# Optimization experiments

Hardware: AMD Instinct MI355X
Metric: run time of the kernel (lower is better)

The kernel has to match this reference:

```python
import jax, jax.numpy as jnp
import numpy as np

TAU = 0.1  # temperature (registered buffer, non-trainable)
EPS = 1e-12  # F.normalize eps


def setup_inputs() -> dict:
    key = jax.random.key(0)
    k1, k2 = jax.random.split(key)
    B, C = 4096, 512
    z1 = jax.random.normal(k1, (B, C), dtype=jnp.float32)
    z2 = jax.random.normal(k2, (B, C), dtype=jnp.float32)
    return {"z1": z1, "z2": z2}


def _l2_normalize(x):
    # matches F.normalize(p=2, dim=1): x / max(||x||, eps)
    n = jnp.sqrt(jnp.sum(x * x, axis=1, keepdims=True))
    return x / jnp.maximum(n, EPS)


def reference(z1, z2):
    B = z1.shape[0]
    N = 2 * B
    z = jnp.concatenate([_l2_normalize(z1), _l2_normalize(z2)], axis=0)  # [2B, C]
    # cosine similarity of unit vectors == dot product -> single GEMM
    S = jnp.exp((z @ z.T) / TAU)  # [2B, 2B]
    rows = jnp.arange(N)
    pos_cols = (rows + B) % N  # mask[r, c]=1 iff r == (c+B) mod 2B  <=> c == (r+B) mod 2B
    positive = S[rows, pos_cols]                 # [2B]
    # negatives = row sum over ~mask; note the original INCLUDES the diagonal
    negative = jnp.sum(S, axis=1) - positive     # [2B]
    pairs_loss = -jnp.log(positive / negative)   # [2B]
    loss = pairs_loss.reshape(2, B).sum(axis=0) / N  # [B]
    return loss.mean()  # reduce=True
```

## Files before the change

### kernel.cpp

```cpp
#include <hip/hip_runtime.h>
#include <hip/hip_bf16.h>


#define BDIM 4096
#define CDIM 512
#define NROWS 8192
#define NTILE 32
#define NBLK 528
#define NKT 8

typedef __attribute__((ext_vector_type(4))) float f32x4;
typedef __attribute__((ext_vector_type(8))) short bf16x8;

#define AS1 __attribute__((address_space(1)))
#define AS3 __attribute__((address_space(3)))

__device__ __forceinline__ unsigned short f2bf_rne(float x) {
    unsigned u = __float_as_uint(x);
    u += 0x7fffu + ((u >> 16) & 1u);
    return (unsigned short)(u >> 16);
}

__global__ __launch_bounds__(256) void normalize_kernel(
    const float* __restrict__ z1, const float* __restrict__ z2,
    unsigned short* __restrict__ zb, float* __restrict__ pos10,
    float* __restrict__ rowsum, float* __restrict__ out) {
    if (blockIdx.x == 0) {
#pragma unroll
        for (int i = 0; i < NROWS / 256; ++i) rowsum[i * 256 + threadIdx.x] = 0.f;
        if (threadIdx.x == 0) out[0] = 0.f;
    }
    const int w = threadIdx.x >> 6, lane = threadIdx.x & 63;
    const int r = blockIdx.x * 4 + w;
    const float4* p1 = (const float4*)(z1 + (size_t)r * CDIM);
    const float4* p2 = (const float4*)(z2 + (size_t)r * CDIM);
    float4 a0 = p1[lane], a1 = p1[64 + lane];
    float4 b0 = p2[lane], b1 = p2[64 + lane];
    float s1 = a0.x * a0.x + a0.y * a0.y + a0.z * a0.z + a0.w * a0.w +
               a1.x * a1.x + a1.y * a1.y + a1.z * a1.z + a1.w * a1.w;
    float s2 = b0.x * b0.x + b0.y * b0.y + b0.z * b0.z + b0.w * b0.w +
               b1.x * b1.x + b1.y * b1.y + b1.z * b1.z + b1.w * b1.w;
    float d = a0.x * b0.x + a0.y * b0.y + a0.z * b0.z + a0.w * b0.w +
              a1.x * b1.x + a1.y * b1.y + a1.z * b1.z + a1.w * b1.w;
#pragma unroll
    for (int m = 1; m < 64; m <<= 1) {
        s1 += __shfl_xor(s1, m, 64);
        s2 += __shfl_xor(s2, m, 64);
        d += __shfl_xor(d, m, 64);
    }
    const float n1 = fmaxf(sqrtf(s1), 1e-12f);
    const float n2 = fmaxf(sqrtf(s2), 1e-12f);
    const float i1 = 1.0f / n1, i2 = 1.0f / n2;
    ushort4 o;
    ushort4* q1 = (ushort4*)(zb + (size_t)r * CDIM);
    ushort4* q2 = (ushort4*)(zb + (size_t)(r + BDIM) * CDIM);
    o.x = f2bf_rne(a0.x * i1); o.y = f2bf_rne(a0.y * i1);
    o.z = f2bf_rne(a0.z * i1); o.w = f2bf_rne(a0.w * i1);
    q1[lane] = o;
    o.x = f2bf_rne(a1.x * i1); o.y = f2bf_rne(a1.y * i1);
    o.z = f2bf_rne(a1.z * i1); o.w = f2bf_rne(a1.w * i1);
    q1[64 + lane] = o;
    o.x = f2bf_rne(b0.x * i2); o.y = f2bf_rne(b0.y * i2);
    o.z = f2bf_rne(b0.z * i2); o.w = f2bf_rne(b0.w * i2);
    q2[lane] = o;
    o.x = f2bf_rne(b1.x * i2); o.y = f2bf_rne(b1.y * i2);
    o.z = f2bf_rne(b1.z * i2); o.w = f2bf_rne(b1.w * i2);
    q2[64 + lane] = o;
    if (lane == 0) pos10[r] = (d / (n1 * n2)) * 10.0f;
}

__global__ __launch_bounds__(512, 2) void simgemm_kernel(
    const unsigned short* __restrict__ Z, float* __restrict__ rowsum) {
    int by = 0, rem = blockIdx.x;
    while (rem >= NTILE - by) { rem -= NTILE - by; ++by; }
    const int bx = by + rem;
    const bool diag = (bx == by);

    __shared__ unsigned short lds[2][4][128 * 64];

    const int t = threadIdx.x;
    const int lane = t & 63, w = t >> 6;
    const int wr = w >> 2, wc = w & 3;

    f32x4 acc[8][4] = {};

    const int srow = t >> 3;
    const int scolb = (((t & 7) ^ ((t >> 3) & 7)) << 4);
    const char* Zb = (const char*)Z;
    const size_t apan = ((size_t)(by * 256) << 10);
    const size_t bpan = ((size_t)(bx * 256) << 10);

#define STG(T, J)                                                                \
    {                                                                            \
        const size_t pb_ = ((J) < 2 ? apan : bpan);                              \
        const char* g0_ = Zb + pb_ +                                             \
            ((size_t)((((J) & 1) * 128) + srow) << 10) + ((T) * 128) + scolb;    \
        char* d0_ = (char*)&lds[(T) & 1][J][0] + w * 1024;                       \
        __builtin_amdgcn_global_load_lds((const AS1 void*)g0_,                   \
                                         (AS3 void*)d0_, 16, 0, 0);              \
        __builtin_amdgcn_global_load_lds((const AS1 void*)(g0_ + (64 << 10)),    \
                                         (AS3 void*)(d0_ + 8192), 16, 0, 0);     \
    }

    STG(0, 2); STG(0, 3); STG(0, 0); STG(0, 1); STG(1, 2); STG(1, 0);
    asm volatile("s_waitcnt vmcnt(4)\n\ts_barrier" ::: "memory");

    const int arow = lane & 15;
    const int brow0 = (wc & 1) * 64;
    const int klo = (lane >> 4) << 4;
    const int swz = (lane & 7) << 4;

#pragma unroll
    for (int T = 0; T < NKT; ++T) {
        const int buf = T & 1;
        const char* Ab = (const char*)&lds[buf][wr][0];
        const char* Bb = (const char*)&lds[buf][2 + (wc >> 1)][0];
        if (T >= 1) {
            if (T < NKT - 1)
                asm volatile("s_waitcnt vmcnt(4)\n\ts_barrier" ::: "memory");
            else
                asm volatile("s_waitcnt vmcnt(0)\n\ts_barrier" ::: "memory");
        }

        bf16x8 af[4][2], bf[4][2];

#pragma unroll
        for (int mi = 0; mi < 4; ++mi)
#pragma unroll
            for (int kk = 0; kk < 2; ++kk)
                af[mi][kk] = *(const bf16x8*)(Ab + (mi * 16 + arow) * 128 +
                                              ((kk * 64 + klo) ^ swz));
#pragma unroll
        for (int ni = 0; ni < 2; ++ni)
#pragma unroll
            for (int kk = 0; kk < 2; ++kk)
                bf[ni][kk] = *(const bf16x8*)(Bb + (brow0 + ni * 16 + arow) * 128 +
                                              ((kk * 64 + klo) ^ swz));
        if (T + 1 < NKT) STG(T + 1, 3);
        asm volatile("s_barrier" ::: "memory");
        __builtin_amdgcn_s_setprio(1);
#pragma unroll
        for (int mi = 0; mi < 4; ++mi)
#pragma unroll
            for (int ni = 0; ni < 2; ++ni)
#pragma unroll
                for (int kk = 0; kk < 2; ++kk)
                    acc[mi][ni] = __builtin_amdgcn_mfma_f32_16x16x32_bf16(
                        af[mi][kk], bf[ni][kk], acc[mi][ni], 0, 0, 0);
        __builtin_amdgcn_s_setprio(0);
        asm volatile("s_waitcnt lgkmcnt(0)\n\ts_barrier" ::: "memory");

#pragma unroll
        for (int ni = 2; ni < 4; ++ni)
#pragma unroll
            for (int kk = 0; kk < 2; ++kk)
                bf[ni][kk] = *(const bf16x8*)(Bb + (brow0 + ni * 16 + arow) * 128 +
                                              ((kk * 64 + klo) ^ swz));
        if (T + 1 < NKT) STG(T + 1, 1);
        asm volatile("s_barrier" ::: "memory");
        __builtin_amdgcn_s_setprio(1);
#pragma unroll
        for (int mi = 0; mi < 4; ++mi)
#pragma unroll
            for (int ni = 2; ni < 4; ++ni)
#pragma unroll
                for (int kk = 0; kk < 2; ++kk)
                    acc[mi][ni] = __builtin_amdgcn_mfma_f32_16x16x32_bf16(
                        af[mi][kk], bf[ni][kk], acc[mi][ni], 0, 0, 0);
        __builtin_amdgcn_s_setprio(0);
        asm volatile("s_waitcnt lgkmcnt(0)\n\ts_barrier" ::: "memory");

#pragma unroll
        for (int mi = 0; mi < 4; ++mi)
#pragma unroll
            for (int kk = 0; kk < 2; ++kk)
                af[mi][kk] = *(const bf16x8*)(Ab + ((mi + 4) * 16 + arow) * 128 +
                                              ((kk * 64 + klo) ^ swz));
        if (T + 2 < NKT) STG(T + 2, 2);
        asm volatile("s_barrier" ::: "memory");
        __builtin_amdgcn_s_setprio(1);
#pragma unroll
        for (int mi = 0; mi < 4; ++mi)
#pragma unroll
            for (int ni = 0; ni < 2; ++ni)
#pragma unroll
                for (int kk = 0; kk < 2; ++kk)
                    acc[mi + 4][ni] = __builtin_amdgcn_mfma_f32_16x16x32_bf16(
                        af[mi][kk], bf[ni][kk], acc[mi + 4][ni], 0, 0, 0);
        __builtin_amdgcn_s_setprio(0);
        asm volatile("s_waitcnt lgkmcnt(0)\n\ts_barrier" ::: "memory");

        if (T + 2 < NKT) STG(T + 2, 0);
        asm volatile("s_barrier" ::: "memory");
        __builtin_amdgcn_s_setprio(1);
#pragma unroll
        for (int mi = 0; mi < 4; ++mi)
#pragma unroll
            for (int ni = 2; ni < 4; ++ni)
#pragma unroll
                for (int kk = 0; kk < 2; ++kk)
                    acc[mi + 4][ni] = __builtin_amdgcn_mfma_f32_16x16x32_bf16(
                        af[mi][kk], bf[ni][kk], acc[mi + 4][ni], 0, 0, 0);
        __builtin_amdgcn_s_setprio(0);
        asm volatile("s_waitcnt lgkmcnt(0)\n\ts_barrier" ::: "memory");
    }
#undef STG

    const float SC = 14.4269504088896340736f;
    const int g = lane >> 4;
    float cs[4] = {0.f, 0.f, 0.f, 0.f};
#pragma unroll
    for (int mi = 0; mi < 8; ++mi) {
        float rs0 = 0.f, rs1 = 0.f, rs2 = 0.f, rs3 = 0.f;
#pragma unroll
        for (int ni = 0; ni < 4; ++ni) {
            f32x4 a = acc[mi][ni];
            const float e0 = exp2f(a[0] * SC);
            const float e1 = exp2f(a[1] * SC);
            const float e2 = exp2f(a[2] * SC);
            const float e3 = exp2f(a[3] * SC);
            rs0 += e0; rs1 += e1; rs2 += e2; rs3 += e3;
            cs[ni] += (e0 + e1) + (e2 + e3);
        }
#pragma unroll
        for (int m = 1; m < 16; m <<= 1) {
            rs0 += __shfl_xor(rs0, m, 64);
            rs1 += __shfl_xor(rs1, m, 64);
            rs2 += __shfl_xor(rs2, m, 64);
            rs3 += __shfl_xor(rs3, m, 64);
        }
        if ((lane & 15) == 0) {
            const int rbase = by * 256 + wr * 128 + mi * 16 + g * 4;
            atomicAdd(&rowsum[rbase + 0], rs0);
            atomicAdd(&rowsum[rbase + 1], rs1);
            atomicAdd(&rowsum[rbase + 2], rs2);
            atomicAdd(&rowsum[rbase + 3], rs3);
        }
    }
    if (!diag) {
#pragma unroll
        for (int ni = 0; ni < 4; ++ni) {
            float c = cs[ni];
            c += __shfl_xor(c, 16, 64);
            c += __shfl_xor(c, 32, 64);
            if (lane < 16)
                atomicAdd(&rowsum[bx * 256 + wc * 64 + ni * 16 + lane], c);
        }
    }
}

__global__ __launch_bounds__(256) void finalize_kernel(
    const float* __restrict__ rowsum, const float* __restrict__ pos10,
    float* __restrict__ out) {
    __shared__ float sm[4];
    const int w = threadIdx.x >> 6, lane = threadIdx.x & 63;
    const int r = blockIdx.x * 256 + threadIdx.x;
    const float p10 = pos10[r];
    const float pos = expf(p10);
    float l = (logf(rowsum[r] - pos) - p10) +
              (logf(rowsum[r + BDIM] - pos) - p10);
#pragma unroll
    for (int m = 1; m < 64; m <<= 1) l += __shfl_xor(l, m, 64);
    if (lane == 0) sm[w] = l;
    __syncthreads();
    if (threadIdx.x == 0) {
        const float tot = sm[0] + sm[1] + sm[2] + sm[3];
        atomicAdd(out, tot * (1.0f / ((float)NROWS * (float)BDIM)));
    }
}

extern "C" void kernel_launch(void* const* d_in, const int* in_sizes, int n_in,
                              void* d_out, int out_size, void* d_ws, size_t ws_size,
                              hipStream_t stream) {
    const float* z1 = (const float*)d_in[0];
    const float* z2 = (const float*)d_in[1];
    float* out = (float*)d_out;
    unsigned short* zb = (unsigned short*)d_ws;
    float* rowsum = (float*)((char*)d_ws + (size_t)NROWS * CDIM * 2);
    float* pos10 = rowsum + NROWS;

    normalize_kernel<<<BDIM / 4, 256, 0, stream>>>(z1, z2, zb, pos10, rowsum, out);
    simgemm_kernel<<<NBLK, 512, 0, stream>>>(zb, rowsum);
    finalize_kernel<<<BDIM / 256, 256, 0, stream>>>(rowsum, pos10, out);
}
```

Measured before the change: 143.3 us.

## Split anti-diagonal tiles into quarter blocks and remap tile order for balance

```diff
diff --git a/kernel.cpp b/kernel.cpp
--- a/kernel.cpp
+++ b/kernel.cpp
@@ -6,8 +6,8 @@
 #define CDIM 512
 #define NROWS 8192
 #define NTILE 32
-#define NBLK 528
 #define NKT 8
+#define NBLK 576
 
 typedef __attribute__((ext_vector_type(4))) float f32x4;
 typedef __attribute__((ext_vector_type(8))) short bf16x8;
@@ -71,24 +71,36 @@
 
 __global__ __launch_bounds__(512, 2) void simgemm_kernel(
     const unsigned short* __restrict__ Z, float* __restrict__ rowsum) {
-    int by = 0, rem = blockIdx.x;
-    while (rem >= NTILE - by) { rem -= NTILE - by; ++by; }
-    const int bx = by + rem;
-    const bool diag = (bx == by);
-
     __shared__ unsigned short lds[2][4][128 * 64];
 
     const int t = threadIdx.x;
     const int lane = t & 63, w = t >> 6;
     const int wr = w >> 2, wc = w & 3;
-
-    f32x4 acc[8][4] = {};
-
     const int srow = t >> 3;
     const int scolb = (((t & 7) ^ ((t >> 3) & 7)) << 4);
     const char* Zb = (const char*)Z;
-    const size_t apan = ((size_t)(by * 256) << 10);
-    const size_t bpan = ((size_t)(bx * 256) << 10);
+    const float SC = 14.4269504088896340736f;
+    const int g = lane >> 4;
+    const int arow = lane & 15;
+    const int klo = (lane >> 4) << 4;
+    const int swz = (lane & 7) << 4;
+    const int bid = blockIdx.x;
+
+    if (bid < 512) {
+        const int fid = (bid & 7) * 64 + (bid >> 3);
+        int by = 0, rem = fid;
+        while (true) {
+            const int cnt = (NTILE - by) - (by <= 15 ? 1 : 0);
+            if (rem < cnt) break;
+            rem -= cnt; ++by;
+        }
+        int bx = by + rem;
+        if (by <= 15 && bx >= 31 - by) ++bx;
+        const bool diag = (bx == by);
+
+        f32x4 acc[8][4] = {};
+        const size_t apan = ((size_t)(by * 256) << 10);
+        const size_t bpan = ((size_t)(bx * 256) << 10);
 
 #define STG(T, J)                                                                \
     {                                                                            \
@@ -102,150 +114,220 @@
                                          (AS3 void*)(d0_ + 8192), 16, 0, 0);     \
     }
 
-    STG(0, 2); STG(0, 3); STG(0, 0); STG(0, 1); STG(1, 2); STG(1, 0);
-    asm volatile("s_waitcnt vmcnt(4)\n\ts_barrier" ::: "memory");
-
-    const int arow = lane & 15;
-    const int brow0 = (wc & 1) * 64;
-    const int klo = (lane >> 4) << 4;
-    const int swz = (lane & 7) << 4;
-
-#pragma unroll
-    for (int T = 0; T < NKT; ++T) {
-        const int buf = T & 1;
-        const char* Ab = (const char*)&lds[buf][wr][0];
-        const char* Bb = (const char*)&lds[buf][2 + (wc >> 1)][0];
-        if (T >= 1) {
-            if (T < NKT - 1)
-                asm volatile("s_waitcnt vmcnt(4)\n\ts_barrier" ::: "memory");
-            else
-                asm volatile("s_waitcnt vmcnt(0)\n\ts_barrier" ::: "memory");
-        }
-
-        bf16x8 af[4][2], bf[4][2];
-
-#pragma unroll
-        for (int mi = 0; mi < 4; ++mi)
-#pragma unroll
-            for (int kk = 0; kk < 2; ++kk)
-                af[mi][kk] = *(const bf16x8*)(Ab + (mi * 16 + arow) * 128 +
-                                              ((kk * 64 + klo) ^ swz));
-#pragma unroll
-        for (int ni = 0; ni < 2; ++ni)
-#pragma unroll
-            for (int kk = 0; kk < 2; ++kk)
-                bf[ni][kk] = *(const bf16x8*)(Bb + (brow0 + ni * 16 + arow) * 128 +
-                                              ((kk * 64 + klo) ^ swz));
-        if (T + 1 < NKT) STG(T + 1, 3);
-        asm volatile("s_barrier" ::: "memory");
-        __builtin_amdgcn_s_setprio(1);
-#pragma unroll
-        for (int mi = 0; mi < 4; ++mi)
+        STG(0, 2); STG(0, 3); STG(0, 0); STG(0, 1); STG(1, 2); STG(1, 0);
+        asm volatile("s_waitcnt vmcnt(4)\n\ts_barrier" ::: "memory");
+
+        const int brow0 = (wc & 1) * 64;
+#pragma unroll
+        for (int T = 0; T < NKT; ++T) {
+            const int buf = T & 1;
+            const char* Ab = (const char*)&lds[buf][wr][0];
+            const char* Bb = (const char*)&lds[buf][2 + (wc >> 1)][0];
+            if (T >= 1) {
+                if (T < NKT - 1)
+                    asm volatile("s_waitcnt vmcnt(4)\n\ts_barrier" ::: "memory");
+                else
+                    asm volatile("s_waitcnt vmcnt(0)\n\ts_barrier" ::: "memory");
+            }
+
+            bf16x8 af[4][2], bf[4][2];
+
+#pragma unroll
+            for (int mi = 0; mi < 4; ++mi)
+#pragma unroll
+                for (int kk = 0; kk < 2; ++kk)
+                    af[mi][kk] = *(const bf16x8*)(Ab + (mi * 16 + arow) * 128 +
+                                                  ((kk * 64 + klo) ^ swz));
 #pragma unroll
             for (int ni = 0; ni < 2; ++ni)
 #pragma unroll
                 for (int kk = 0; kk < 2; ++kk)
-                    acc[mi][ni] = __builtin_amdgcn_mfma_f32_16x16x32_bf16(
-                        af[mi][kk], bf[ni][kk], acc[mi][ni], 0, 0, 0);
-        __builtin_amdgcn_s_setprio(0);
-        asm volatile("s_waitcnt lgkmcnt(0)\n\ts_barrier" ::: "memory");
-
-#pragma unroll
-        for (int ni = 2; ni < 4; ++ni)
-#pragma unroll
-            for (int kk = 0; kk < 2; ++kk)
-                bf[ni][kk] = *(const bf16x8*)(Bb + (brow0 + ni * 16 + arow) * 128 +
-                                              ((kk * 64 + klo) ^ swz));
-        if (T + 1 < NKT) STG(T + 1, 1);
-        asm volatile("s_barrier" ::: "memory");
-        __builtin_amdgcn_s_setprio(1);
-#pragma unroll
-        for (int mi = 0; mi < 4; ++mi)
+                    bf[ni][kk] = *(const bf16x8*)(Bb + (brow0 + ni * 16 + arow) * 128 +
+                                                  ((kk * 64 + klo) ^ swz));
+            if (T + 1 < NKT) STG(T + 1, 3);
+            asm volatile("s_barrier" ::: "memory");
+            __builtin_amdgcn_s_setprio(1);
+#pragma unroll
+            for (int mi = 0; mi < 4; ++mi)
+#pragma unroll
+                for (int ni = 0; ni < 2; ++ni)
+#pragma unroll
+                    for (int kk = 0; kk < 2; ++kk)
+                        acc[mi][ni] = __builtin_amdgcn_mfma_f32_16x16x32_bf16(
+                            af[mi][kk], bf[ni][kk], acc[mi][ni], 0, 0, 0);
+            __builtin_amdgcn_s_setprio(0);
+            asm volatile("s_waitcnt lgkmcnt(0)\n\ts_barrier" ::: "memory");
+
 #pragma unroll
             for (int ni = 2; ni < 4; ++ni)
 #pragma unroll
                 for (int kk = 0; kk < 2; ++kk)
-                    acc[mi][ni] = __builtin_amdgcn_mfma_f32_16x16x32_bf16(
-                        af[mi][kk], bf[ni][kk], acc[mi][ni], 0, 0, 0);
-        __builtin_amdgcn_s_setprio(0);
-        asm volatile("s_waitcnt lgkmcnt(0)\n\ts_barrier" ::: "memory");
-
-#pragma unroll
-        for (int mi = 0; mi < 4; ++mi)
-#pragma unroll
-            for (int kk = 0; kk < 2; ++kk)
-                af[mi][kk] = *(const bf16x8*)(Ab + ((mi + 4) * 16 + arow) * 128 +
-                                              ((kk * 64 + klo) ^ swz));
-        if (T + 2 < NKT) STG(T + 2, 2);
-        asm volatile("s_barrier" ::: "memory");
-        __builtin_amdgcn_s_setprio(1);
-#pragma unroll
-        for (int mi = 0; mi < 4; ++mi)
-#pragma unroll
-            for (int ni = 0; ni < 2; ++ni)
+                    bf[ni][kk] = *(const bf16x8*)(Bb + (brow0 + ni * 16 + arow) * 128 +
+                                                  ((kk * 64 + klo) ^ swz));
+            if (T + 1 < NKT) STG(T + 1, 1);
+            asm volatile("s_barrier" ::: "memory");
+            __builtin_amdgcn_s_setprio(1);
+#pragma unroll
+            for (int mi = 0; mi < 4; ++mi)
+#pragma unroll
+                for (int ni = 2; ni < 4; ++ni)
+#pragma unroll
+                    for (int kk = 0; kk < 2; ++kk)
+                        acc[mi][ni] = __builtin_amdgcn_mfma_f32_16x16x32_bf16(
+                            af[mi][kk], bf[ni][kk], acc[mi][ni], 0, 0, 0);
+            __builtin_amdgcn_s_setprio(0);
+            asm volatile("s_waitcnt lgkmcnt(0)\n\ts_barrier" ::: "memory");
+
+#pragma unroll
+            for (int mi = 0; mi < 4; ++mi)
 #pragma unroll
                 for (int kk = 0; kk < 2; ++kk)
-                    acc[mi + 4][ni] = __builtin_amdgcn_mfma_f32_16x16x32_bf16(
-                        af[mi][kk], bf[ni][kk], acc[mi + 4][ni], 0, 0, 0);
-        __builtin_amdgcn_s_setprio(0);
-        asm volatile("s_waitcnt lgkmcnt(0)\n\ts_barrier" ::: "memory");
-
-        if (T + 2 < NKT) STG(T + 2, 0);
-        asm volatile("s_barrier" ::: "memory");
-        __builtin_amdgcn_s_setprio(1);
-#pragma unroll
-        for (int mi = 0; mi < 4; ++mi)
-#pragma unroll
-            for (int ni = 2; ni < 4; ++ni)
-#pragma unroll
-                for (int kk = 0; kk < 2; ++kk)
-                    acc[mi + 4][ni] = __builtin_amdgcn_mfma_f32_16x16x32_bf16(
-                        af[mi][kk], bf[ni][kk], acc[mi + 4][ni], 0, 0, 0);
-        __builtin_amdgcn_s_setprio(0);
-        asm volatile("s_waitcnt lgkmcnt(0)\n\ts_barrier" ::: "memory");
-    }
+                    af[mi][kk] = *(const bf16x8*)(Ab + ((mi + 4) * 16 + arow) * 128 +
+                                                  ((kk * 64 + klo) ^ swz));
+            if (T + 2 < NKT) STG(T + 2, 2);
+            asm volatile("s_barrier" ::: "memory");
+            __builtin_amdgcn_s_setprio(1);
+#pragma unroll
+            for (int mi = 0; mi < 4; ++mi)
+#pragma unroll
+                for (int ni = 0; ni < 2; ++ni)
+#pragma unroll
+                    for (int kk = 0; kk < 2; ++kk)
+                        acc[mi + 4][ni] = __builtin_amdgcn_mfma_f32_16x16x32_bf16(
+                            af[mi][kk], bf[ni][kk], acc[mi + 4][ni], 0, 0, 0);
+            __builtin_amdgcn_s_setprio(0);
+            asm volatile("s_waitcnt lgkmcnt(0)\n\ts_barrier" ::: "memory");
+
+            if (T + 2 < NKT) STG(T + 2, 0);
+            asm volatile("s_barrier" ::: "memory");
+            __builtin_amdgcn_s_setprio(1);
+#pragma unroll
+            for (int mi = 0; mi < 4; ++mi)
+#pragma unroll
+                for (int ni = 2; ni < 4; ++ni)
+#pragma unroll
+                    for (int kk = 0; kk < 2; ++kk)
+                        acc[mi + 4][ni] = __builtin_amdgcn_mfma_f32_16x16x32_bf16(
+                            af[mi][kk], bf[ni][kk], acc[mi + 4][ni], 0, 0, 0);
+            __builtin_amdgcn_s_setprio(0);
+            asm volatile("s_waitcnt lgkmcnt(0)\n\ts_barrier" ::: "memory");
+        }
 #undef STG
 
-    const float SC = 14.4269504088896340736f;
-    const int g = lane >> 4;
-    float cs[4] = {0.f, 0.f, 0.f, 0.f};
-#pragma unroll
-    for (int mi = 0; mi < 8; ++mi) {
-        float rs0 = 0.f, rs1 = 0.f, rs2 = 0.f, rs3 = 0.f;
-#pragma unroll
-        for (int ni = 0; ni < 4; ++ni) {
-            f32x4 a = acc[mi][ni];
+        float cs[4] = {0.f, 0.f, 0.f, 0.f};
+#pragma unroll
+        for (int mi = 0; mi < 8; ++mi) {
+            float rs0 = 0.f, rs1 = 0.f, rs2 = 0.f, rs3 = 0.f;
+#pragma unroll
+            for (int ni = 0; ni < 4; ++ni) {
+                f32x4 a = acc[mi][ni];
+                const float e0 = exp2f(a[0] * SC);
+                const float e1 = exp2f(a[1] * SC);
+                const float e2 = exp2f(a[2] * SC);
+                const float e3 = exp2f(a[3] * SC);
+                rs0 += e0; rs1 += e1; rs2 += e2; rs3 += e3;
+                cs[ni] += (e0 + e1) + (e2 + e3);
+            }
+#pragma unroll
+            for (int m = 1; m < 16; m <<= 1) {
+                rs0 += __shfl_xor(rs0, m, 64);
+                rs1 += __shfl_xor(rs1, m, 64);
+                rs2 += __shfl_xor(rs2, m, 64);
+                rs3 += __shfl_xor(rs3, m, 64);
+            }
+            if ((lane & 15) == 0) {
+                const int rbase = by * 256 + wr * 128 + mi * 16 + g * 4;
+                atomicAdd(&rowsum[rbase + 0], rs0);
+                atomicAdd(&rowsum[rbase + 1], rs1);
+                atomicAdd(&rowsum[rbase + 2], rs2);
+                atomicAdd(&rowsum[rbase + 3], rs3);
+            }
+        }
+        if (!diag) {
+#pragma unroll
+            for (int ni = 0; ni < 4; ++ni) {
+                float c = cs[ni];
+                c += __shfl_xor(c, 16, 64);
+                c += __shfl_xor(c, 32, 64);
+                if (lane < 16)
+                    atomicAdd(&rowsum[bx * 256 + wc * 64 + ni * 16 + lane], c);
+            }
+        }
+    } else {
+        const int qi = bid - 512;
+        const int by = qi >> 2, bx = 31 - (qi >> 2), cq = qi & 3;
+        const size_t apan = ((size_t)(by * 256) << 10);
+        const size_t bq = ((size_t)(bx * 256 + cq * 64) << 10);
+
+        f32x4 accq[8] = {};
+
+#define GLD(gp, dp) __builtin_amdgcn_global_load_lds((const AS1 void*)(gp), (AS3 void*)(dp), 16, 0, 0)
+#define STGQ(T, d)                                                               \
+    {                                                                            \
+        _Pragma("unroll") for (int J_ = 0; J_ < 2; ++J_) {                       \
+            const char* g0_ = Zb + apan +                                        \
+                ((size_t)(J_ * 128 + srow) << 10) + ((T) << 7) + scolb;          \
+            char* d0_ = (char*)&lds[d][J_][0] + w * 1024;                        \
+            GLD(g0_, d0_);                                                       \
+            GLD(g0_ + (64 << 10), d0_ + 8192);                                   \
+        }                                                                        \
+        GLD(Zb + bq + ((size_t)srow << 10) + ((T) << 7) + scolb,                 \
+            (char*)&lds[d][2][0] + w * 1024);                                    \
+    }
+
+        STGQ(0, 0);
+        __syncthreads();
+#pragma unroll
+        for (int T = 0; T < NKT; ++T) {
+            const int d = T & 1;
+            if (T < NKT - 1) STGQ(T + 1, d ^ 1);
+            const char* Aw = (const char*)&lds[d][wr][0];
+            const char* Bq = (const char*)&lds[d][2][0];
+#pragma unroll
+            for (int kk = 0; kk < 2; ++kk) {
+                const int koff = (kk * 64 + klo) ^ swz;
+                bf16x8 bfq = *(const bf16x8*)(Bq + (wc * 16 + arow) * 128 + koff);
+#pragma unroll
+                for (int mi = 0; mi < 8; ++mi) {
+                    bf16x8 afm = *(const bf16x8*)(Aw + (mi * 16 + arow) * 128 + koff);
+                    accq[mi] = __builtin_amdgcn_mfma_f32_16x16x32_bf16(
+                        afm, bfq, accq[mi], 0, 0, 0);
+                }
+            }
+            __syncthreads();
+        }
+#undef STGQ
+#undef GLD
+
+        float cs = 0.f;
+#pragma unroll
+        for (int mi = 0; mi < 8; ++mi) {
+            f32x4 a = accq[mi];
             const float e0 = exp2f(a[0] * SC);
             const float e1 = exp2f(a[1] * SC);
             const float e2 = exp2f(a[2] * SC);
             const float e3 = exp2f(a[3] * SC);
-            rs0 += e0; rs1 += e1; rs2 += e2; rs3 += e3;
-            cs[ni] += (e0 + e1) + (e2 + e3);
-        }
-#pragma unroll
-        for (int m = 1; m < 16; m <<= 1) {
-            rs0 += __shfl_xor(rs0, m, 64);
-            rs1 += __shfl_xor(rs1, m, 64);
-            rs2 += __shfl_xor(rs2, m, 64);
-            rs3 += __shfl_xor(rs3, m, 64);
-        }
-        if ((lane & 15) == 0) {
-            const int rbase = by * 256 + wr * 128 + mi * 16 + g * 4;
-            atomicAdd(&rowsum[rbase + 0], rs0);
-            atomicAdd(&rowsum[rbase + 1], rs1);
-            atomicAdd(&rowsum[rbase + 2], rs2);
-            atomicAdd(&rowsum[rbase + 3], rs3);
-        }
-    }
-    if (!diag) {
-#pragma unroll
-        for (int ni = 0; ni < 4; ++ni) {
-            float c = cs[ni];
-            c += __shfl_xor(c, 16, 64);
-            c += __shfl_xor(c, 32, 64);
-            if (lane < 16)
-                atomicAdd(&rowsum[bx * 256 + wc * 64 + ni * 16 + lane], c);
-        }
+            float rs0 = e0, rs1 = e1, rs2 = e2, rs3 = e3;
+            cs += (e0 + e1) + (e2 + e3);
+#pragma unroll
+            for (int m = 1; m < 16; m <<= 1) {
+                rs0 += __shfl_xor(rs0, m, 64);
+                rs1 += __shfl_xor(rs1, m, 64);
+                rs2 += __shfl_xor(rs2, m, 64);
+                rs3 += __shfl_xor(rs3, m, 64);
+            }
+            if ((lane & 15) == 0) {
+                const int rbase = by * 256 + wr * 128 + mi * 16 + g * 4;
+                atomicAdd(&rowsum[rbase + 0], rs0);
+                atomicAdd(&rowsum[rbase + 1], rs1);
+                atomicAdd(&rowsum[rbase + 2], rs2);
+                atomicAdd(&rowsum[rbase + 3], rs3);
+            }
+        }
+        cs += __shfl_xor(cs, 16, 64);
+        cs += __shfl_xor(cs, 32, 64);
+        if (lane < 16)
+            atomicAdd(&rowsum[bx * 256 + cq * 64 + wc * 16 + lane], cs);
     }
 }
 
```

Result: faster. 139.0 us (-3.0%).
